# Kernel tuning notes

Hardware: AMD Instinct MI355X
Metric: run time of the kernel (lower is better)

## Reference

```python
import jax, jax.numpy as jnp
import numpy as np

K = 512
DIM = 64


def setup_inputs() -> dict:
    key = jax.random.key(0)
    kx, ke = jax.random.split(key)
    x = jax.random.normal(kx, (64, 64, 32, 32), dtype=jnp.float32)  # (b, d, h, w)
    codebook = jax.random.normal(ke, (K, DIM), dtype=jnp.float32)  # nn.Embedding weight
    return {"x": x, "codebook": codebook}


def reference(x, codebook):
    b, d, h, w = x.shape
    # (b, d, h*w) -> (b, h*w, d)
    flat = jnp.transpose(x.reshape(b, d, h * w), (0, 2, 1))  # (b, n, d)
    x2 = jnp.sum(flat * flat, axis=-1, keepdims=True)              # (b, n, 1)
    e2 = jnp.sum(codebook * codebook, axis=-1)                     # (k,)
    xe = jnp.einsum('bnd,kd->bnk', flat, codebook)                 # (b, n, k)
    dist = x2 - 2.0 * xe + e2                                      # (b, n, k)
    idx = jnp.argmin(dist, axis=-1)                                # (b, n)
    quant = codebook[idx]                                          # (b, n, d) gather
    # straight-through estimator
    quant_st = flat + jax.lax.stop_gradient(quant - flat)
    out = jnp.transpose(quant_st, (0, 2, 1)).reshape(b, d, h, w)
    return out
```

## Files before the change

### kernel.cpp

```cpp
#include <hip/hip_runtime.h>

#define KCODES 512
#define DIM    64
#define NVEC   65536
#define TAU    0.05f

typedef __attribute__((ext_vector_type(8))) short   short8;
typedef __attribute__((ext_vector_type(4))) float   f32x4;

static __device__ __forceinline__ unsigned f2bfu(float f) {
    unsigned u = __builtin_bit_cast(unsigned, f);
    u += 0x7fffu + ((u >> 16) & 1u);
    return u >> 16;
}

__global__ void prep_kernel(const float* __restrict__ cb,
                            unsigned short* __restrict__ cbt,
                            float* __restrict__ e2q) {
    if (blockIdx.x < 128) {
        const int g   = blockIdx.x * 64 + threadIdx.x;
        const int s   = g >> 10;
        const int rem = g & 1023;
        const int h   = rem >> 9;
        const int qd  = (rem >> 6) & 7;
        const int cl  = rem & 63;
        const float* src = cb + (size_t)(s * 64 + cl) * DIM + qd * 8;
        short8 v;
#pragma unroll
        for (int j = 0; j < 8; ++j) {
            float f = src[j];
            unsigned u = __builtin_bit_cast(unsigned, f);
            if (h == 0) {
                v[j] = (short)(u >> 16);
            } else {
                float hi = __builtin_bit_cast(float, u & 0xFFFF0000u);
                v[j] = (short)f2bfu(f - hi);
            }
        }
        *(short8*)(cbt + (size_t)g * 8) = v;
    } else {
        const int k = blockIdx.x - 128;
        float v = cb[k * DIM + threadIdx.x];
        double p = (double)v * (double)v;
#pragma unroll
        for (int off = 32; off > 0; off >>= 1) p += __shfl_down(p, off, 64);
        if (threadIdx.x == 0) e2q[k] = (float)(0.5 * p + 256.0);
    }
}

__launch_bounds__(256, 4)
__global__ void vq_main(const float* __restrict__ x,
                        const float* __restrict__ cb,
                        const unsigned short* __restrict__ cbt,
                        const float* __restrict__ e2q,
                        float* __restrict__ out) {
    __shared__ __align__(16) unsigned short sA[2][8192];
    __shared__ float sE2[KCODES];
    __shared__ int   s_i1[64], s_i2[64], s_flag[64], s_win[64];

    const int tid  = threadIdx.x;
    const int wave = tid >> 6;
    const int lane = tid & 63;
    const int quad = lane >> 4;
    const int l16  = lane & 15;

    const int v0    = blockIdx.x * 64;
    const int b     = v0 >> 10;
    const int nbase = v0 & 1023;
    const float* xb = x + (size_t)b * 65536;

    short8 stg[4];
#pragma unroll
    for (int r = 0; r < 4; ++r)
        stg[r] = *(const short8*)(cbt + (size_t)(tid + r * 256) * 8);

    short8 Bh[2], Bl[2];
    {
        const int n_g = nbase + wave * 16 + l16;
#pragma unroll
        for (int ko = 0; ko < 2; ++ko) {
#pragma unroll
            for (int j = 0; j < 8; ++j) {
                const int d = quad * 8 + j + ko * 32;
                float f = -xb[(size_t)d * 1024 + n_g];
                unsigned u = __builtin_bit_cast(unsigned, f);
                float hi = __builtin_bit_cast(float, u & 0xFFFF0000u);
                Bh[ko][j] = (short)(u >> 16);
                Bl[ko][j] = (short)f2bfu(f - hi);
            }
        }
    }

    if (tid < 128) *(f32x4*)(sE2 + tid * 4) = *(const f32x4*)(e2q + tid * 4);
#pragma unroll
    for (int r = 0; r < 4; ++r)
        *(short8*)(sA[0] + (size_t)(tid + r * 256) * 8) = stg[r];
    __syncthreads();

    float f1 = 1e30f, f2_ = 1e30f;
    int   i1 = 0,     i2_ = 0;

#pragma unroll 1
    for (int s = 0; s < 8; ++s) {
        if (s < 7) {
#pragma unroll
            for (int r = 0; r < 4; ++r)
                stg[r] = *(const short8*)(cbt +
                          (size_t)((s + 1) * 1024 + tid + r * 256) * 8);
        }

        const unsigned short* buf = sA[s & 1];
#pragma unroll
        for (int st = 0; st < 4; ++st) {
            const int cbase = s * 64 + st * 16;
            const int roff  = quad * 64 + st * 16 + l16;
            short8 A00 = *(const short8*)(buf + (size_t)(      roff) * 8);
            short8 A01 = *(const short8*)(buf + (size_t)(256 + roff) * 8);
            short8 A10 = *(const short8*)(buf + (size_t)(512 + roff) * 8);
            short8 A11 = *(const short8*)(buf + (size_t)(768 + roff) * 8);
            f32x4  e2v = *(const f32x4*)(sE2 + cbase + quad * 4);

            f32x4 acc = e2v;
            acc = __builtin_amdgcn_mfma_f32_16x16x32_bf16(A00, Bh[0], acc, 0, 0, 0);
            acc = __builtin_amdgcn_mfma_f32_16x16x32_bf16(A01, Bh[1], acc, 0, 0, 0);
            acc = __builtin_amdgcn_mfma_f32_16x16x32_bf16(A00, Bl[0], acc, 0, 0, 0);
            acc = __builtin_amdgcn_mfma_f32_16x16x32_bf16(A01, Bl[1], acc, 0, 0, 0);
            acc = __builtin_amdgcn_mfma_f32_16x16x32_bf16(A10, Bh[0], acc, 0, 0, 0);
            acc = __builtin_amdgcn_mfma_f32_16x16x32_bf16(A11, Bh[1], acc, 0, 0, 0);

#pragma unroll
            for (int r = 0; r < 4; ++r) {
                float dd = acc[r];
                int   id = cbase + quad * 4 + r;
                bool  c1 = dd < f1;
                bool  c2 = dd < f2_;
                i2_ = c1 ? i1 : (c2 ? id : i2_);
                f2_ = fminf(fmaxf(f1, dd), f2_);
                i1  = c1 ? id : i1;
                f1  = fminf(f1, dd);
            }
        }

        if (s < 7) {
#pragma unroll
            for (int r = 0; r < 4; ++r)
                *(short8*)(sA[(s + 1) & 1] + (size_t)(tid + r * 256) * 8) = stg[r];
        }
        __syncthreads();
    }

    {
#pragma unroll
        for (int delta = 16; delta <= 32; delta <<= 1) {
            float of1 = __shfl_xor(f1, delta, 64);
            int   oi1 = __shfl_xor(i1, delta, 64);
            float of2 = __shfl_xor(f2_, delta, 64);
            int   oi2 = __shfl_xor(i2_, delta, 64);
            bool o1_first = (of1 < f1) || (of1 == f1 && oi1 < i1);
            if (o1_first) {
                bool keep = (f1 < of2) || (f1 == of2 && i1 < oi2);
                f2_ = keep ? f1 : of2;
                i2_ = keep ? i1 : oi2;
                f1 = of1; i1 = oi1;
            } else {
                bool o1_second = (of1 < f2_) || (of1 == f2_ && oi1 < i2_);
                if (o1_second) { f2_ = of1; i2_ = oi1; }
            }
        }
        if (quad == 0) {
            const int vl = wave * 16 + l16;
            s_win[vl]  = i1;
            s_i1[vl]   = i1;
            s_i2[vl]   = i2_;
            s_flag[vl] = (f2_ - f1) < TAU;
        }
    }
    __syncthreads();

    {
        const int vec = tid >> 2, sub = tid & 3;
        if (s_flag[vec]) {
            const int i1c = s_i1[vec], i2c = s_i2[vec];
            const float* xr = xb + nbase + vec;
            const float* r1 = cb + (size_t)i1c * DIM;
            const float* r2 = cb + (size_t)i2c * DIM;
            double D1 = 0.0, D2 = 0.0;
#pragma unroll 4
            for (int i = 0; i < 16; ++i) {
                const int d = sub + 4 * i;
                double xd = (double)xr[(size_t)d * 1024];
                double t1 = xd - (double)r1[d]; D1 += t1 * t1;
                double t2 = xd - (double)r2[d]; D2 += t2 * t2;
            }
            D1 += __shfl_down(D1, 2, 64); D1 += __shfl_down(D1, 1, 64);
            D2 += __shfl_down(D2, 2, 64); D2 += __shfl_down(D2, 1, 64);
            if (sub == 0) {
                if (D2 < D1 || (D2 == D1 && i2c < i1c)) s_win[vec] = i2c;
            }
        }
    }
    __syncthreads();

    {
        const int n    = tid & 63;
        const int dgrp = tid >> 6;
        const float4* crow = (const float4*)(cb + (size_t)s_win[n] * DIM);
        float* op = out + (size_t)b * 65536 + nbase + n;
#pragma unroll
        for (int i = 0; i < 4; ++i) {
            const int d0 = dgrp * 16 + i * 4;
            float4 val = crow[d0 >> 2];
            op[(size_t)(d0 + 0) * 1024] = val.x;
            op[(size_t)(d0 + 1) * 1024] = val.y;
            op[(size_t)(d0 + 2) * 1024] = val.z;
            op[(size_t)(d0 + 3) * 1024] = val.w;
        }
    }
}

extern "C" void kernel_launch(void* const* d_in, const int* in_sizes, int n_in,
                              void* d_out, int out_size, void* d_ws, size_t ws_size,
                              hipStream_t stream) {
    const float* x  = (const float*)d_in[0];
    const float* cb = (const float*)d_in[1];
    float* out = (float*)d_out;

    unsigned short* cbt = (unsigned short*)d_ws;
    float*          e2q = (float*)(cbt + 8192 * 8);

    prep_kernel<<<640, 64, 0, stream>>>(cb, cbt, e2q);
    vq_main<<<NVEC / 64, 256, 0, stream>>>(x, cb, cbt, e2q, out);
}
```

Before: 90.94 us.

## Stage whole codebook in LDS with 1024-thread blocks of 256 vectors

```diff
diff --git a/kernel.cpp b/kernel.cpp
--- a/kernel.cpp
+++ b/kernel.cpp
@@ -48,15 +48,15 @@
     }
 }
 
-__launch_bounds__(256, 4)
+__launch_bounds__(1024, 4)
 __global__ void vq_main(const float* __restrict__ x,
                         const float* __restrict__ cb,
                         const unsigned short* __restrict__ cbt,
                         const float* __restrict__ e2q,
                         float* __restrict__ out) {
-    __shared__ __align__(16) unsigned short sA[2][8192];
+    __shared__ __align__(16) unsigned short sA[65536];
     __shared__ float sE2[KCODES];
-    __shared__ int   s_i1[64], s_i2[64], s_flag[64], s_win[64];
+    __shared__ int   s_i1[256], s_i2[256], s_flag[256], s_win[256];
 
     const int tid  = threadIdx.x;
     const int wave = tid >> 6;
@@ -64,15 +64,15 @@
     const int quad = lane >> 4;
     const int l16  = lane & 15;
 
-    const int v0    = blockIdx.x * 64;
+    const int v0    = blockIdx.x * 256;
     const int b     = v0 >> 10;
     const int nbase = v0 & 1023;
     const float* xb = x + (size_t)b * 65536;
 
-    short8 stg[4];
-#pragma unroll
-    for (int r = 0; r < 4; ++r)
-        stg[r] = *(const short8*)(cbt + (size_t)(tid + r * 256) * 8);
+    short8 stg[8];
+#pragma unroll
+    for (int r = 0; r < 8; ++r)
+        stg[r] = *(const short8*)(cbt + (size_t)(tid + r * 1024) * 8);
 
     short8 Bh[2], Bl[2];
     {
@@ -93,60 +93,44 @@
 
     if (tid < 128) *(f32x4*)(sE2 + tid * 4) = *(const f32x4*)(e2q + tid * 4);
 #pragma unroll
-    for (int r = 0; r < 4; ++r)
-        *(short8*)(sA[0] + (size_t)(tid + r * 256) * 8) = stg[r];
+    for (int r = 0; r < 8; ++r)
+        *(short8*)(sA + (size_t)(tid + r * 1024) * 8) = stg[r];
     __syncthreads();
 
     float f1 = 1e30f, f2_ = 1e30f;
     int   i1 = 0,     i2_ = 0;
 
-#pragma unroll 1
-    for (int s = 0; s < 8; ++s) {
-        if (s < 7) {
-#pragma unroll
-            for (int r = 0; r < 4; ++r)
-                stg[r] = *(const short8*)(cbt +
-                          (size_t)((s + 1) * 1024 + tid + r * 256) * 8);
-        }
-
-        const unsigned short* buf = sA[s & 1];
-#pragma unroll
-        for (int st = 0; st < 4; ++st) {
-            const int cbase = s * 64 + st * 16;
-            const int roff  = quad * 64 + st * 16 + l16;
-            short8 A00 = *(const short8*)(buf + (size_t)(      roff) * 8);
-            short8 A01 = *(const short8*)(buf + (size_t)(256 + roff) * 8);
-            short8 A10 = *(const short8*)(buf + (size_t)(512 + roff) * 8);
-            short8 A11 = *(const short8*)(buf + (size_t)(768 + roff) * 8);
-            f32x4  e2v = *(const f32x4*)(sE2 + cbase + quad * 4);
-
-            f32x4 acc = e2v;
-            acc = __builtin_amdgcn_mfma_f32_16x16x32_bf16(A00, Bh[0], acc, 0, 0, 0);
-            acc = __builtin_amdgcn_mfma_f32_16x16x32_bf16(A01, Bh[1], acc, 0, 0, 0);
-            acc = __builtin_amdgcn_mfma_f32_16x16x32_bf16(A00, Bl[0], acc, 0, 0, 0);
-            acc = __builtin_amdgcn_mfma_f32_16x16x32_bf16(A01, Bl[1], acc, 0, 0, 0);
-            acc = __builtin_amdgcn_mfma_f32_16x16x32_bf16(A10, Bh[0], acc, 0, 0, 0);
-            acc = __builtin_amdgcn_mfma_f32_16x16x32_bf16(A11, Bh[1], acc, 0, 0, 0);
-
-#pragma unroll
-            for (int r = 0; r < 4; ++r) {
-                float dd = acc[r];
-                int   id = cbase + quad * 4 + r;
-                bool  c1 = dd < f1;
-                bool  c2 = dd < f2_;
-                i2_ = c1 ? i1 : (c2 ? id : i2_);
-                f2_ = fminf(fmaxf(f1, dd), f2_);
-                i1  = c1 ? id : i1;
-                f1  = fminf(f1, dd);
-            }
-        }
-
-        if (s < 7) {
-#pragma unroll
-            for (int r = 0; r < 4; ++r)
-                *(short8*)(sA[(s + 1) & 1] + (size_t)(tid + r * 256) * 8) = stg[r];
-        }
-        __syncthreads();
+#pragma unroll 2
+    for (int sg = 0; sg < 32; ++sg) {
+        const int s     = sg >> 2;
+        const int st    = sg & 3;
+        const int cbase = sg * 16;
+        const int g0    = s * 1024 + quad * 64 + st * 16 + l16;
+        short8 A00 = *(const short8*)(sA + (size_t)(g0      ) * 8);
+        short8 A01 = *(const short8*)(sA + (size_t)(g0 + 256) * 8);
+        short8 A10 = *(const short8*)(sA + (size_t)(g0 + 512) * 8);
+        short8 A11 = *(const short8*)(sA + (size_t)(g0 + 768) * 8);
+        f32x4  e2v = *(const f32x4*)(sE2 + cbase + quad * 4);
+
+        f32x4 acc = e2v;
+        acc = __builtin_amdgcn_mfma_f32_16x16x32_bf16(A00, Bh[0], acc, 0, 0, 0);
+        acc = __builtin_amdgcn_mfma_f32_16x16x32_bf16(A01, Bh[1], acc, 0, 0, 0);
+        acc = __builtin_amdgcn_mfma_f32_16x16x32_bf16(A00, Bl[0], acc, 0, 0, 0);
+        acc = __builtin_amdgcn_mfma_f32_16x16x32_bf16(A01, Bl[1], acc, 0, 0, 0);
+        acc = __builtin_amdgcn_mfma_f32_16x16x32_bf16(A10, Bh[0], acc, 0, 0, 0);
+        acc = __builtin_amdgcn_mfma_f32_16x16x32_bf16(A11, Bh[1], acc, 0, 0, 0);
+
+#pragma unroll
+        for (int r = 0; r < 4; ++r) {
+            float dd = acc[r];
+            int   id = cbase + quad * 4 + r;
+            bool  c1 = dd < f1;
+            bool  c2 = dd < f2_;
+            i2_ = c1 ? i1 : (c2 ? id : i2_);
+            f2_ = fminf(fmaxf(f1, dd), f2_);
+            i1  = c1 ? id : i1;
+            f1  = fminf(f1, dd);
+        }
     }
 
     {
@@ -202,8 +186,8 @@
     __syncthreads();
 
     {
-        const int n    = tid & 63;
-        const int dgrp = tid >> 6;
+        const int n    = tid & 255;
+        const int dgrp = tid >> 8;
         const float4* crow = (const float4*)(cb + (size_t)s_win[n] * DIM);
         float* op = out + (size_t)b * 65536 + nbase + n;
 #pragma unroll
@@ -229,5 +213,5 @@
     float*          e2q = (float*)(cbt + 8192 * 8);
 
     prep_kernel<<<640, 64, 0, stream>>>(cb, cbt, e2q);
-    vq_main<<<NVEC / 64, 256, 0, stream>>>(x, cb, cbt, e2q, out);
-}
+    vq_main<<<NVEC / 256, 1024, 0, stream>>>(x, cb, cbt, e2q, out);
+}
```

New measurement: 93.81 us. 1.03x slower.
